# Kernel optimization log

Measured on AMD Instinct MI355X. Metric: run time of the kernel, lower is better.

## Reference

```python
import jax, jax.numpy as jnp
import numpy as np

N = 50000      # nodes
E = 800000     # edges (avg degree 16)
F_IN = 128
HID = 128
C = 40
EPS = 1e-5     # BatchNorm1d eps


def setup_inputs() -> dict:
    key = jax.random.key(0)
    ks = jax.random.split(key, 8)

    def glorot(k, shape):
        lim = np.sqrt(6.0 / (shape[0] + shape[1])).astype(np.float32)
        return jax.random.uniform(k, shape, jnp.float32, -lim, lim)

    inp = {
        "features": jax.random.normal(ks[0], (N, F_IN), jnp.float32),
        "edge_index": jax.random.randint(ks[1], (2, E), 0, N, jnp.int32),
        "W1": glorot(ks[2], (F_IN, HID)), "b1": jnp.zeros((HID,), jnp.float32),
        "gamma1": jnp.ones((HID,), jnp.float32), "beta1": jnp.zeros((HID,), jnp.float32),
        "W2": glorot(ks[3], (HID, HID)), "b2": jnp.zeros((HID,), jnp.float32),
        "gamma2": jnp.ones((HID,), jnp.float32), "beta2": jnp.zeros((HID,), jnp.float32),
        "W3": glorot(ks[4], (HID, C)), "b3": jnp.zeros((C,), jnp.float32),
    }
    return inp


def _gcn_norm(edge_index):
    # Add self-loops and compute symmetric normalization D^-1/2 (A+I) D^-1/2
    loops = jnp.arange(N, dtype=edge_index.dtype)
    src = jnp.concatenate([edge_index[0], loops])
    dst = jnp.concatenate([edge_index[1], loops])
    deg = jax.ops.segment_sum(jnp.ones((E + N,), jnp.float32), dst, num_segments=N)
    dinv = jax.lax.rsqrt(jnp.maximum(deg, 1.0))
    return src, dst, dinv[src] * dinv[dst]  # per-edge norm coefficient


def _gcn_conv(x, W, b, src, dst, norm):
    h = x @ W                                   # [N, out]
    msg = h[src] * norm[:, None]                # gather + scale, [E+N, out]
    return jax.ops.segment_sum(msg, dst, num_segments=N) + b


def _bn(x, gamma, beta):
    # training-mode BatchNorm1d over the node axis (biased variance)
    mu = jnp.mean(x, axis=0)
    var = jnp.mean(jnp.square(x - mu), axis=0)
    return (x - mu) * jax.lax.rsqrt(var + EPS) * gamma + beta


def reference(features, edge_index, W1, b1, gamma1, beta1, W2, b2, gamma2, beta2, W3, b3):
    src, dst, norm = _gcn_norm(edge_index)
    h = jax.nn.relu(_bn(_gcn_conv(features, W1, b1, src, dst, norm), gamma1, beta1))
    h = jax.nn.relu(_bn(_gcn_conv(h, W2, b2, src, dst, norm), gamma2, beta2))
    h = _gcn_conv(h, W3, b3, src, dst, norm)
    return jax.nn.log_softmax(h, axis=-1)
```

## Files before the change

kernel.cpp:

```cpp
#include <hip/hip_runtime.h>
#include <math.h>

#define FEAT 128
#define NCLS 40
#define BN_EPS 1e-5f
#define CAP 64

typedef unsigned short u16;
typedef unsigned int u32;
typedef __attribute__((ext_vector_type(8))) short bf16x8;
typedef __attribute__((ext_vector_type(4))) float f32x4;

__device__ inline u32 f2b2(float a, float b) {
    u32 ua = __float_as_uint(a), ub = __float_as_uint(b);
    ua = (ua + 0x7fffu + ((ua >> 16) & 1u)) >> 16;
    ub = (ub + 0x7fffu + ((ub >> 16) & 1u)) >> 16;
    return ua | (ub << 16);
}
__device__ inline u16 f2b1(float a) {
    u32 ua = __float_as_uint(a);
    return (u16)((ua + 0x7fffu + ((ua >> 16) & 1u)) >> 16);
}
__device__ inline float b2f(u16 u) { return __uint_as_float((u32)u << 16); }
__device__ inline float blo(u32 u) { return __uint_as_float(u << 16); }
__device__ inline float bhi(u32 u) { return __uint_as_float(u & 0xffff0000u); }

__device__ inline void b8acc(uint4 u, float w, float* a) {
    a[0] = fmaf(w, blo(u.x), a[0]); a[1] = fmaf(w, bhi(u.x), a[1]);
    a[2] = fmaf(w, blo(u.y), a[2]); a[3] = fmaf(w, bhi(u.y), a[3]);
    a[4] = fmaf(w, blo(u.z), a[4]); a[5] = fmaf(w, bhi(u.z), a[5]);
    a[6] = fmaf(w, blo(u.w), a[6]); a[7] = fmaf(w, bhi(u.w), a[7]);
}


__device__ inline void stage_wt(const float* __restrict__ W, u16* Wt) {
    const float4* W4 = (const float4*)W;
#pragma unroll
    for (int i = 0; i < 16; ++i) {
        int li = threadIdx.x + i * 256;
        int k = li >> 5;
        int n0 = (li & 31) * 4;
        int s = k >> 5, quad = (k >> 3) & 3, koff = k & 7;
        int nt = n0 >> 4, nl0 = n0 & 15;
        int base = ((s * 8 + nt) * 64 + quad * 16) * 8 + koff;
        float4 w = W4[li];
        Wt[base + (nl0 + 0) * 8] = f2b1(w.x);
        Wt[base + (nl0 + 1) * 8] = f2b1(w.y);
        Wt[base + (nl0 + 2) * 8] = f2b1(w.z);
        Wt[base + (nl0 + 3) * 8] = f2b1(w.w);
    }
}

__device__ inline void stage_wt40(const float* __restrict__ W, u16* Wt) {
    for (int e = threadIdx.x; e < 12 * 64 * 8; e += 256) {
        int j = e & 7;
        int lane = (e >> 3) & 63;
        int tile = e >> 9;
        int s = tile / 3, nt = tile % 3;
        int n = nt * 16 + (lane & 15);
        int k = s * 32 + (lane >> 4) * 8 + j;
        float v = (n < NCLS) ? W[k * NCLS + n] : 0.f;
        Wt[e] = f2b1(v);
    }
}

__global__ __launch_bounds__(256) void k_init(
    const float* __restrict__ W1, const float* __restrict__ W2,
    const float* __restrict__ W3, u16* __restrict__ Wg,
    uint4* __restrict__ zbase, int zcount, int zblocks,
    const int* __restrict__ edges, u16* __restrict__ ew, int twoE)
{
    int b = blockIdx.x;
    if (b == 0) stage_wt(W1, Wg);
    else if (b == 1) stage_wt(W2, Wg + 128 * 128);
    else if (b == 2) stage_wt40(W3, Wg + 2 * 128 * 128);
    else if (b < 3 + zblocks) {
        int idx = (b - 3) * 256 + threadIdx.x;
        if (idx < zcount) zbase[idx] = make_uint4(0, 0, 0, 0);
    } else {
        int idx = ((b - 3 - zblocks) * 256 + threadIdx.x) * 8;
        if (idx + 8 <= twoE) {
            int4 a = *(const int4*)(edges + idx);
            int4 c = *(const int4*)(edges + idx + 4);
            uint4 o;
            o.x = (u32)(a.x & 0xffff) | ((u32)a.y << 16);
            o.y = (u32)(a.z & 0xffff) | ((u32)a.w << 16);
            o.z = (u32)(c.x & 0xffff) | ((u32)c.y << 16);
            o.w = (u32)(c.z & 0xffff) | ((u32)c.w << 16);
            *(uint4*)(ew + idx) = o;
        } else {
            for (int e = idx; e < twoE; ++e) ew[e] = (u16)edges[e];
        }
    }
}

__device__ inline void mfma_core(const uint4* __restrict__ wt4, const bf16x8* bfrag,
                                 u16* __restrict__ Y, int node, int M, int nl, int quad) {
    int lane = quad * 16 + nl;
    f32x4 acc[8];
#pragma unroll
    for (int nt = 0; nt < 8; ++nt) acc[nt] = (f32x4){0.f, 0.f, 0.f, 0.f};
#pragma unroll
    for (int s = 0; s < 4; ++s) {
#pragma unroll
        for (int nt = 0; nt < 8; ++nt) {
            uint4 aw = wt4[(s * 8 + nt) * 64 + lane];
            bf16x8 af = *(bf16x8*)&aw;
            acc[nt] = __builtin_amdgcn_mfma_f32_16x16x32_bf16(af, bfrag[s], acc[nt], 0, 0, 0);
        }
    }
    if (node < M) {
#pragma unroll
        for (int nt = 0; nt < 8; ++nt) {
            uint2 o;
            o.x = f2b2(acc[nt][0], acc[nt][1]);
            o.y = f2b2(acc[nt][2], acc[nt][3]);
            *(uint2*)&Y[(size_t)node * 128 + nt * 16 + quad * 4] = o;
        }
    }
}


__global__ __launch_bounds__(256, 8) void k_l1_fill(
    const float* __restrict__ X, const u16* __restrict__ Wg, u16* __restrict__ Y, int M,
    const u16* __restrict__ srcw, const u16* __restrict__ dstw,
    int* __restrict__ cnt, u16* __restrict__ col, int E,
    int gemmBlocks, int nchunks)
{
    if ((int)blockIdx.x < gemmBlocks) {
        int wv = threadIdx.x >> 6;
        int lane = threadIdx.x & 63;
        int nl = lane & 15, quad = lane >> 4;
        int node = blockIdx.x * 64 + wv * 16 + nl;

        bf16x8 bfrag[4];
        if (node < M) {
            const float4* xr = (const float4*)(X + (size_t)node * 128);
#pragma unroll
            for (int s = 0; s < 4; ++s) {
                float4 xa = xr[s * 8 + quad * 2];
                float4 xb = xr[s * 8 + quad * 2 + 1];
                uint4 bu;
                bu.x = f2b2(xa.x, xa.y); bu.y = f2b2(xa.z, xa.w);
                bu.z = f2b2(xb.x, xb.y); bu.w = f2b2(xb.z, xb.w);
                bfrag[s] = *(bf16x8*)&bu;
            }
        } else {
            uint4 z = make_uint4(0, 0, 0, 0);
#pragma unroll
            for (int s = 0; s < 4; ++s) bfrag[s] = *(bf16x8*)&z;
        }
        mfma_core((const uint4*)Wg, bfrag, Y, node, M, nl, quad);
    } else {
        int fb = blockIdx.x - gemmBlocks;
        int part = fb & 7;
        int chunk = fb >> 3;
        int lo = (int)(((long long)M * part) >> 3);
        int hi = (int)(((long long)M * (part + 1)) >> 3);
        int per = ((E + nchunks - 1) / nchunks + 7) & ~7;
        int e0 = chunk * per;
        int e1 = e0 + per; if (e1 > E) e1 = E;

        for (int eb = e0 + (int)threadIdx.x * 8; eb < e1; eb += 2048) {
            if (eb + 8 <= e1) {
                uint4 du = *(const uint4*)(dstw + eb);
                uint4 su = *(const uint4*)(srcw + eb);
                int dd[8] = {(int)(du.x & 0xffffu), (int)(du.x >> 16),
                             (int)(du.y & 0xffffu), (int)(du.y >> 16),
                             (int)(du.z & 0xffffu), (int)(du.z >> 16),
                             (int)(du.w & 0xffffu), (int)(du.w >> 16)};
                u16 ss[8] = {(u16)(su.x & 0xffffu), (u16)(su.x >> 16),
                             (u16)(su.y & 0xffffu), (u16)(su.y >> 16),
                             (u16)(su.z & 0xffffu), (u16)(su.z >> 16),
                             (u16)(su.w & 0xffffu), (u16)(su.w >> 16)};
#pragma unroll
                for (int k = 0; k < 8; ++k) {
                    int d = dd[k];
                    if (d >= lo && d < hi) {
                        int c = atomicAdd(&cnt[d], 1);
                        if (c < CAP) col[(size_t)d * CAP + c] = ss[k];
                    }
                }
            } else {
                for (int e = eb; e < e1; ++e) {
                    int d = (int)dstw[e];
                    if (d >= lo && d < hi) {
                        int c = atomicAdd(&cnt[d], 1);
                        if (c < CAP) col[(size_t)d * CAP + c] = srcw[e];
                    }
                }
            }
        }
    }
}


__device__ inline void build_bfrag_bn(const u16* __restrict__ X, int node, int M,
                                      int quad, const float* scs, const float* shs,
                                      bf16x8* bfrag) {
    if (node < M) {
        const uint4* xr = (const uint4*)(X + (size_t)node * 128);
#pragma unroll
        for (int s = 0; s < 4; ++s) {
            int k0 = s * 32 + quad * 8;
            uint4 xu = xr[s * 4 + quad];
            float4 sc0 = *(const float4*)&scs[k0];
            float4 sc1 = *(const float4*)&scs[k0 + 4];
            float4 sh0 = *(const float4*)&shs[k0];
            float4 sh1 = *(const float4*)&shs[k0 + 4];
            float v0 = fmaxf(fmaf(blo(xu.x), sc0.x, sh0.x), 0.f);
            float v1 = fmaxf(fmaf(bhi(xu.x), sc0.y, sh0.y), 0.f);
            float v2 = fmaxf(fmaf(blo(xu.y), sc0.z, sh0.z), 0.f);
            float v3 = fmaxf(fmaf(bhi(xu.y), sc0.w, sh0.w), 0.f);
            float v4 = fmaxf(fmaf(blo(xu.z), sc1.x, sh1.x), 0.f);
            float v5 = fmaxf(fmaf(bhi(xu.z), sc1.y, sh1.y), 0.f);
            float v6 = fmaxf(fmaf(blo(xu.w), sc1.z, sh1.z), 0.f);
            float v7 = fmaxf(fmaf(bhi(xu.w), sc1.w, sh1.w), 0.f);
            uint4 bu;
            bu.x = f2b2(v0, v1); bu.y = f2b2(v2, v3);
            bu.z = f2b2(v4, v5); bu.w = f2b2(v6, v7);
            bfrag[s] = *(bf16x8*)&bu;
        }
    } else {
        uint4 z = make_uint4(0, 0, 0, 0);
#pragma unroll
        for (int s = 0; s < 4; ++s) bfrag[s] = *(bf16x8*)&z;
    }
}

__global__ __launch_bounds__(256, 2) void k_mfma_l2(
    const u16* __restrict__ X, const u16* __restrict__ Wg,
    const float* __restrict__ sums, const float* __restrict__ gamma,
    const float* __restrict__ beta, u16* __restrict__ Y, int M)
{
    __shared__ __align__(16) u16 Wt[128 * 128];
    __shared__ __align__(16) float scs[128], shs[128];

    if (threadIdx.x < 128) {
        int f = threadIdx.x;
        float inv_n = 1.f / (float)M;
        float mu = sums[f] * inv_n;
        float var = sums[128 + f] * inv_n - mu * mu;
        float rs = rsqrtf(var + BN_EPS);
        float sc = gamma[f] * rs;
        scs[f] = sc;
        shs[f] = beta[f] - mu * sc;
    }
    {
        uint4* d4 = (uint4*)Wt;
        const uint4* s4 = (const uint4*)Wg;
#pragma unroll
        for (int i = 0; i < 8; ++i) d4[threadIdx.x + i * 256] = s4[threadIdx.x + i * 256];
    }
    __syncthreads();

    int wv = threadIdx.x >> 6;
    int lane = threadIdx.x & 63;
    int nl = lane & 15, quad = lane >> 4;
    int nodeA = blockIdx.x * 128 + wv * 16 + nl;
    int nodeB = nodeA + 64;

    bf16x8 bfragA[4], bfragB[4];
    build_bfrag_bn(X, nodeA, M, quad, scs, shs, bfragA);
    build_bfrag_bn(X, nodeB, M, quad, scs, shs, bfragB);

    const uint4* wt4 = (const uint4*)Wt;
    f32x4 accA[8], accB[8];
#pragma unroll
    for (int nt = 0; nt < 8; ++nt) {
        accA[nt] = (f32x4){0.f, 0.f, 0.f, 0.f};
        accB[nt] = (f32x4){0.f, 0.f, 0.f, 0.f};
    }
#pragma unroll
    for (int s = 0; s < 4; ++s) {
#pragma unroll
        for (int nt = 0; nt < 8; ++nt) {
            uint4 aw = wt4[(s * 8 + nt) * 64 + lane];
            bf16x8 af = *(bf16x8*)&aw;
            accA[nt] = __builtin_amdgcn_mfma_f32_16x16x32_bf16(af, bfragA[s], accA[nt], 0, 0, 0);
            accB[nt] = __builtin_amdgcn_mfma_f32_16x16x32_bf16(af, bfragB[s], accB[nt], 0, 0, 0);
        }
    }
    if (nodeA < M) {
#pragma unroll
        for (int nt = 0; nt < 8; ++nt) {
            uint2 o;
            o.x = f2b2(accA[nt][0], accA[nt][1]);
            o.y = f2b2(accA[nt][2], accA[nt][3]);
            *(uint2*)&Y[(size_t)nodeA * 128 + nt * 16 + quad * 4] = o;
        }
    }
    if (nodeB < M) {
#pragma unroll
        for (int nt = 0; nt < 8; ++nt) {
            uint2 o;
            o.x = f2b2(accB[nt][0], accB[nt][1]);
            o.y = f2b2(accB[nt][2], accB[nt][3]);
            *(uint2*)&Y[(size_t)nodeB * 128 + nt * 16 + quad * 4] = o;
        }
    }
}


__global__ __launch_bounds__(256) void k_mfma_l3(
    const u16* __restrict__ X, const u16* __restrict__ Wg,
    const float* __restrict__ sums, const float* __restrict__ gamma,
    const float* __restrict__ beta, u16* __restrict__ Y, int M)
{
    __shared__ __align__(16) u16 Wt[12 * 64 * 8];
    __shared__ __align__(16) float scs[128], shs[128];

    if (threadIdx.x < 128) {
        int f = threadIdx.x;
        float inv_n = 1.f / (float)M;
        float mu = sums[f] * inv_n;
        float var = sums[128 + f] * inv_n - mu * mu;
        float rs = rsqrtf(var + BN_EPS);
        float sc = gamma[f] * rs;
        scs[f] = sc;
        shs[f] = beta[f] - mu * sc;
    }
    {
        uint4* d4 = (uint4*)Wt;
        const uint4* s4 = (const uint4*)Wg;
#pragma unroll
        for (int i = 0; i < 3; ++i) d4[threadIdx.x + i * 256] = s4[threadIdx.x + i * 256];
    }
    __syncthreads();

    int wv = threadIdx.x >> 6;
    int lane = threadIdx.x & 63;
    int nl = lane & 15, quad = lane >> 4;
    int node = blockIdx.x * 64 + wv * 16 + nl;

    bf16x8 bfrag[4];
    build_bfrag_bn(X, node, M, quad, scs, shs, bfrag);

    const uint4* wt4 = (const uint4*)Wt;
    f32x4 acc[3];
#pragma unroll
    for (int nt = 0; nt < 3; ++nt) acc[nt] = (f32x4){0.f, 0.f, 0.f, 0.f};
#pragma unroll
    for (int s = 0; s < 4; ++s) {
#pragma unroll
        for (int nt = 0; nt < 3; ++nt) {
            uint4 aw = wt4[(s * 3 + nt) * 64 + lane];
            bf16x8 af = *(bf16x8*)&aw;
            acc[nt] = __builtin_amdgcn_mfma_f32_16x16x32_bf16(af, bfrag[s], acc[nt], 0, 0, 0);
        }
    }
    if (node < M) {
#pragma unroll
        for (int nt = 0; nt < 3; ++nt) {
            int c0 = nt * 16 + quad * 4;
            if (c0 < NCLS) {
                uint2 o;
                o.x = f2b2(acc[nt][0], acc[nt][1]);
                o.y = f2b2(acc[nt][2], acc[nt][3]);
                *(uint2*)&Y[(size_t)node * NCLS + c0] = o;
            }
        }
    }
}


__global__ __launch_bounds__(256) void k_agg128_bn(
    const u16* __restrict__ t, const int* __restrict__ cnt,
    const u16* __restrict__ col, const float* __restrict__ bias,
    u16* __restrict__ out, float* __restrict__ sums, int n)
{
    int wid = threadIdx.x >> 4;
    int lane = threadIdx.x & 15;
    float4 bA = ((const float4*)bias)[lane * 2];
    float4 bB = ((const float4*)bias)[lane * 2 + 1];

    float bs[8], bq[8];
#pragma unroll
    for (int k = 0; k < 8; ++k) { bs[k] = 0.f; bq[k] = 0.f; }

    for (int i0 = blockIdx.x * 16; i0 < n; i0 += gridDim.x * 16) {
        int i = i0 + wid;
        if (i < n) {
            int c = cnt[i];
            int deg = c < CAP ? c : CAP;
            int beg = i * CAP, end = beg + deg;
            float di = rsqrtf((float)(c + 1));

            float a[8];
            {
                uint4 su = ((const uint4*)(t + (size_t)i * 128))[lane];
                a[0] = di * blo(su.x); a[1] = di * bhi(su.x);
                a[2] = di * blo(su.y); a[3] = di * bhi(su.y);
                a[4] = di * blo(su.z); a[5] = di * bhi(su.z);
                a[6] = di * blo(su.w); a[7] = di * bhi(su.w);
            }

            int j = beg;
            for (; j + 7 < end; j += 8) {
                int s[8]; int sc[8]; uint4 v[8];
#pragma unroll
                for (int k = 0; k < 8; ++k) s[k] = (int)col[j + k];
#pragma unroll
                for (int k = 0; k < 8; ++k) {
                    sc[k] = cnt[s[k]];
                    v[k] = ((const uint4*)(t + (size_t)s[k] * 128))[lane];
                }
#pragma unroll
                for (int k = 0; k < 8; ++k) b8acc(v[k], rsqrtf((float)(sc[k] + 1)), a);
            }
            for (; j < end; ++j) {
                int s0 = (int)col[j];
                float w0 = rsqrtf((float)(cnt[s0] + 1));
                uint4 v = ((const uint4*)(t + (size_t)s0 * 128))[lane];
                b8acc(v, w0, a);
            }

            float vv[8];
            vv[0] = fmaf(di, a[0], bA.x); vv[1] = fmaf(di, a[1], bA.y);
            vv[2] = fmaf(di, a[2], bA.z); vv[3] = fmaf(di, a[3], bA.w);
            vv[4] = fmaf(di, a[4], bB.x); vv[5] = fmaf(di, a[5], bB.y);
            vv[6] = fmaf(di, a[6], bB.z); vv[7] = fmaf(di, a[7], bB.w);
            uint4 o;
            o.x = f2b2(vv[0], vv[1]); o.y = f2b2(vv[2], vv[3]);
            o.z = f2b2(vv[4], vv[5]); o.w = f2b2(vv[6], vv[7]);
            ((uint4*)(out + (size_t)i * 128))[lane] = o;
#pragma unroll
            for (int k = 0; k < 8; ++k) {
                bs[k] += vv[k];
                bq[k] = fmaf(vv[k], vv[k], bq[k]);
            }
        }
    }

    __shared__ float red[16][128];
#pragma unroll
    for (int k = 0; k < 8; ++k) red[wid][lane * 8 + k] = bs[k];
    __syncthreads();
    if (threadIdx.x < 128) {
        float v = 0.f;
#pragma unroll
        for (int w = 0; w < 16; ++w) v += red[w][threadIdx.x];
        atomicAdd(&sums[threadIdx.x], v);
    }
    __syncthreads();
#pragma unroll
    for (int k = 0; k < 8; ++k) red[wid][lane * 8 + k] = bq[k];
    __syncthreads();
    if (threadIdx.x < 128) {
        float v = 0.f;
#pragma unroll
        for (int w = 0; w < 16; ++w) v += red[w][threadIdx.x];
        atomicAdd(&sums[128 + threadIdx.x], v);
    }
}


__global__ __launch_bounds__(256) void k_agg40(
    const u16* __restrict__ t, const int* __restrict__ cnt,
    const u16* __restrict__ col, const float* __restrict__ bias,
    float* __restrict__ out, int n)
{
    int i = blockIdx.x * 32 + (threadIdx.x >> 3);
    if (i >= n) return;
    int l = threadIdx.x & 7;
    bool act = l < 5;
    int c = cnt[i];
    int deg = c < CAP ? c : CAP;
    int beg = i * CAP, end = beg + deg;
    float di = rsqrtf((float)(c + 1));

    float a[8] = {0.f, 0.f, 0.f, 0.f, 0.f, 0.f, 0.f, 0.f};
    if (act) {
        uint4 su = ((const uint4*)(t + (size_t)i * NCLS))[l];
        a[0] = di * blo(su.x); a[1] = di * bhi(su.x);
        a[2] = di * blo(su.y); a[3] = di * bhi(su.y);
        a[4] = di * blo(su.z); a[5] = di * bhi(su.z);
        a[6] = di * blo(su.w); a[7] = di * bhi(su.w);
    }
    int j = beg;
    for (; j + 7 < end; j += 8) {
        int s[8]; int sc[8]; uint4 v[8];
#pragma unroll
        for (int k = 0; k < 8; ++k) s[k] = (int)col[j + k];
#pragma unroll
        for (int k = 0; k < 8; ++k) {
            sc[k] = cnt[s[k]];
            v[k] = act ? ((const uint4*)(t + (size_t)s[k] * NCLS))[l]
                       : make_uint4(0, 0, 0, 0);
        }
#pragma unroll
        for (int k = 0; k < 8; ++k) b8acc(v[k], rsqrtf((float)(sc[k] + 1)), a);
    }
    for (; j < end; ++j) {
        int s0 = (int)col[j];
        float w0 = rsqrtf((float)(cnt[s0] + 1));
        uint4 v = act ? ((const uint4*)(t + (size_t)s0 * NCLS))[l]
                      : make_uint4(0, 0, 0, 0);
        b8acc(v, w0, a);
    }

    float v[8];
    float m = -INFINITY;
    if (act) {
        float4 b0 = *(const float4*)(bias + l * 8);
        float4 b1 = *(const float4*)(bias + l * 8 + 4);
        v[0] = fmaf(di, a[0], b0.x); v[1] = fmaf(di, a[1], b0.y);
        v[2] = fmaf(di, a[2], b0.z); v[3] = fmaf(di, a[3], b0.w);
        v[4] = fmaf(di, a[4], b1.x); v[5] = fmaf(di, a[5], b1.y);
        v[6] = fmaf(di, a[6], b1.z); v[7] = fmaf(di, a[7], b1.w);
#pragma unroll
        for (int k = 0; k < 8; ++k) m = fmaxf(m, v[k]);
    }
#pragma unroll
    for (int d = 1; d < 8; d <<= 1) m = fmaxf(m, __shfl_xor(m, d, 8));
    float es = 0.f;
    if (act) {
#pragma unroll
        for (int k = 0; k < 8; ++k) es += expf(v[k] - m);
    }
#pragma unroll
    for (int d = 1; d < 8; d <<= 1) es += __shfl_xor(es, d, 8);
    float ls = logf(es);
    if (act) {
        float4 o0, o1;
        o0.x = v[0] - m - ls; o0.y = v[1] - m - ls;
        o0.z = v[2] - m - ls; o0.w = v[3] - m - ls;
        o1.x = v[4] - m - ls; o1.y = v[5] - m - ls;
        o1.z = v[6] - m - ls; o1.w = v[7] - m - ls;
        *(float4*)(out + (size_t)i * NCLS + l * 8) = o0;
        *(float4*)(out + (size_t)i * NCLS + l * 8 + 4) = o1;
    }
}


extern "C" void kernel_launch(void* const* d_in, const int* in_sizes, int n_in,
                              void* d_out, int out_size, void* d_ws, size_t ws_size,
                              hipStream_t stream) {
    const float* features = (const float*)d_in[0];
    const int* edge_index = (const int*)d_in[1];
    const float* W1 = (const float*)d_in[2];
    const float* b1 = (const float*)d_in[3];
    const float* gamma1 = (const float*)d_in[4];
    const float* beta1 = (const float*)d_in[5];
    const float* W2 = (const float*)d_in[6];
    const float* b2 = (const float*)d_in[7];
    const float* gamma2 = (const float*)d_in[8];
    const float* beta2 = (const float*)d_in[9];
    const float* W3 = (const float*)d_in[10];
    const float* b3 = (const float*)d_in[11];
    float* out = (float*)d_out;

    int n = in_sizes[0] / FEAT;
    int E = in_sizes[1] / 2;

    char* p = (char*)d_ws;
    auto alloc = [&](size_t bytes) -> void* {
        void* r = (void*)p;
        p += (bytes + 255) & ~(size_t)255;
        return r;
    };
    int* cnt     = (int*)alloc((size_t)n * 4);
    float* sums  = (float*)alloc(512 * 4);
    size_t zspan = (size_t)((char*)(sums + 512) - (char*)cnt);
    u16* colb    = (u16*)alloc((size_t)n * CAP * 2);
    u16* hb      = (u16*)alloc((size_t)n * 128 * 2);
    u16* ab      = (u16*)alloc((size_t)n * 128 * 2);
    u16* wgb     = (u16*)alloc((size_t)(2 * 128 * 128 + 12 * 64 * 8) * 2);
    u16* ew      = (u16*)alloc((size_t)2 * E * 2);

    float* sums1 = sums;
    float* sums2 = sums + 256;
    u16* Wg1 = wgb;
    u16* Wg2 = wgb + 128 * 128;
    u16* Wg3 = wgb + 2 * 128 * 128;
    u16* srcw = ew;
    u16* dstw = ew + E;

    int gb64 = (n + 63) / 64;
    int gb128 = (n + 127) / 128;
    int gb16 = (n + 15) / 16;
    int gb32 = (n + 31) / 32;
    int aggGrid = gb16 < 1024 ? gb16 : 1024;

    int zcount = (int)(zspan / 16);
    int zblocks = (zcount + 255) / 256;
    int twoE = 2 * E;
    int cblocks = (twoE / 8 + 255) / 256;
    k_init<<<3 + zblocks + cblocks, 256, 0, stream>>>(W1, W2, W3, wgb,
                                                      (uint4*)cnt, zcount, zblocks,
                                                      edge_index, ew, twoE);

    int nchunks = 160;
    k_l1_fill<<<gb64 + nchunks * 8, 256, 0, stream>>>(features, Wg1, hb, n,
                                                      srcw, dstw, cnt, colb, E,
                                                      gb64, nchunks);

    k_agg128_bn<<<aggGrid, 256, 0, stream>>>(hb, cnt, colb, b1, ab, sums1, n);

    k_mfma_l2<<<gb128, 256, 0, stream>>>(ab, Wg2, sums1, gamma1, beta1, hb, n);
    k_agg128_bn<<<aggGrid, 256, 0, stream>>>(hb, cnt, colb, b2, ab, sums2, n);

    k_mfma_l3<<<gb64, 256, 0, stream>>>(ab, Wg3, sums2, gamma2, beta2, hb, n);
    k_agg40<<<gb32, 256, 0, stream>>>(hb, cnt, colb, b3, out, n);
}
```

Measured before the change: 298.6 us.

## Partition aggregation into XCD-local node ranges and batch neighbor-index loads

Both aggregation kernels now map each block to one of eight contiguous node partitions, selected by blockIdx mod 8. The apparent aim is that blocks on the same XCD work on nearby nodes, improving L2 locality for cnt and column reads. The gather loop loads 16 neighbor indices per iteration as two vector loads and unrolls 16 row gathers to raise memory-level parallelism. The tail is handled with masked 8-wide vector loads, which needs 64 bytes of padding on the column buffer. k_agg40 becomes a persistent grid-stride kernel with 512 blocks, and launch bounds now request 4 blocks per CU, which risks register pressure from the 16-deep unroll.

```diff
diff --git a/kernel.cpp b/kernel.cpp
--- a/kernel.cpp
+++ b/kernel.cpp
@@ -364,7 +364,7 @@
 }
 
 
-__global__ __launch_bounds__(256) void k_agg128_bn(
+__global__ __launch_bounds__(256, 4) void k_agg128_bn(
     const u16* __restrict__ t, const int* __restrict__ cnt,
     const u16* __restrict__ col, const float* __restrict__ bias,
     u16* __restrict__ out, float* __restrict__ sums, int n)
@@ -378,9 +378,15 @@
 #pragma unroll
     for (int k = 0; k < 8; ++k) { bs[k] = 0.f; bq[k] = 0.f; }
 
-    for (int i0 = blockIdx.x * 16; i0 < n; i0 += gridDim.x * 16) {
+    int part = blockIdx.x & 7;
+    int bslot = blockIdx.x >> 3;
+    int nb = gridDim.x >> 3;
+    int plo = (int)(((long long)n * part) >> 3);
+    int phi = (int)(((long long)n * (part + 1)) >> 3);
+
+    for (int i0 = plo + bslot * 16; i0 < phi; i0 += nb * 16) {
         int i = i0 + wid;
-        if (i < n) {
+        if (i < phi) {
             int c = cnt[i];
             int deg = c < CAP ? c : CAP;
             int beg = i * CAP, end = beg + deg;
@@ -396,23 +402,45 @@
             }
 
             int j = beg;
-            for (; j + 7 < end; j += 8) {
-                int s[8]; int sc[8]; uint4 v[8];
-#pragma unroll
-                for (int k = 0; k < 8; ++k) s[k] = (int)col[j + k];
-#pragma unroll
-                for (int k = 0; k < 8; ++k) {
+            for (; j + 15 < end; j += 16) {
+                uint4 c0 = *(const uint4*)(col + j);
+                uint4 c1 = *(const uint4*)(col + j + 8);
+                int s[16] = {
+                    (int)(c0.x & 0xffffu), (int)(c0.x >> 16),
+                    (int)(c0.y & 0xffffu), (int)(c0.y >> 16),
+                    (int)(c0.z & 0xffffu), (int)(c0.z >> 16),
+                    (int)(c0.w & 0xffffu), (int)(c0.w >> 16),
+                    (int)(c1.x & 0xffffu), (int)(c1.x >> 16),
+                    (int)(c1.y & 0xffffu), (int)(c1.y >> 16),
+                    (int)(c1.z & 0xffffu), (int)(c1.z >> 16),
+                    (int)(c1.w & 0xffffu), (int)(c1.w >> 16)};
+                int sc[16]; uint4 v[16];
+#pragma unroll
+                for (int k = 0; k < 16; ++k) {
                     sc[k] = cnt[s[k]];
                     v[k] = ((const uint4*)(t + (size_t)s[k] * 128))[lane];
                 }
 #pragma unroll
-                for (int k = 0; k < 8; ++k) b8acc(v[k], rsqrtf((float)(sc[k] + 1)), a);
-            }
-            for (; j < end; ++j) {
-                int s0 = (int)col[j];
-                float w0 = rsqrtf((float)(cnt[s0] + 1));
-                uint4 v = ((const uint4*)(t + (size_t)s0 * 128))[lane];
-                b8acc(v, w0, a);
+                for (int k = 0; k < 16; ++k) b8acc(v[k], rsqrtf((float)(sc[k] + 1)), a);
+            }
+            for (; j < end; j += 8) {
+                uint4 c0 = *(const uint4*)(col + j);
+                int sr[8] = {
+                    (int)(c0.x & 0xffffu), (int)(c0.x >> 16),
+                    (int)(c0.y & 0xffffu), (int)(c0.y >> 16),
+                    (int)(c0.z & 0xffffu), (int)(c0.z >> 16),
+                    (int)(c0.w & 0xffffu), (int)(c0.w >> 16)};
+                float w[8]; uint4 v[8];
+#pragma unroll
+                for (int k = 0; k < 8; ++k) {
+                    bool valid = (j + k) < end;
+                    int s = valid ? sr[k] : 0;
+                    int sck = cnt[s];
+                    v[k] = ((const uint4*)(t + (size_t)s * 128))[lane];
+                    w[k] = valid ? rsqrtf((float)(sck + 1)) : 0.f;
+                }
+#pragma unroll
+                for (int k = 0; k < 8; ++k) b8acc(v[k], w[k], a);
             }
 
             float vv[8];
@@ -455,80 +483,110 @@
 }
 
 
-__global__ __launch_bounds__(256) void k_agg40(
+__global__ __launch_bounds__(256, 4) void k_agg40(
     const u16* __restrict__ t, const int* __restrict__ cnt,
     const u16* __restrict__ col, const float* __restrict__ bias,
     float* __restrict__ out, int n)
 {
-    int i = blockIdx.x * 32 + (threadIdx.x >> 3);
-    if (i >= n) return;
+    int wid = threadIdx.x >> 3;
     int l = threadIdx.x & 7;
     bool act = l < 5;
-    int c = cnt[i];
-    int deg = c < CAP ? c : CAP;
-    int beg = i * CAP, end = beg + deg;
-    float di = rsqrtf((float)(c + 1));
-
-    float a[8] = {0.f, 0.f, 0.f, 0.f, 0.f, 0.f, 0.f, 0.f};
-    if (act) {
-        uint4 su = ((const uint4*)(t + (size_t)i * NCLS))[l];
-        a[0] = di * blo(su.x); a[1] = di * bhi(su.x);
-        a[2] = di * blo(su.y); a[3] = di * bhi(su.y);
-        a[4] = di * blo(su.z); a[5] = di * bhi(su.z);
-        a[6] = di * blo(su.w); a[7] = di * bhi(su.w);
-    }
-    int j = beg;
-    for (; j + 7 < end; j += 8) {
-        int s[8]; int sc[8]; uint4 v[8];
-#pragma unroll
-        for (int k = 0; k < 8; ++k) s[k] = (int)col[j + k];
-#pragma unroll
-        for (int k = 0; k < 8; ++k) {
-            sc[k] = cnt[s[k]];
-            v[k] = act ? ((const uint4*)(t + (size_t)s[k] * NCLS))[l]
-                       : make_uint4(0, 0, 0, 0);
-        }
-#pragma unroll
-        for (int k = 0; k < 8; ++k) b8acc(v[k], rsqrtf((float)(sc[k] + 1)), a);
-    }
-    for (; j < end; ++j) {
-        int s0 = (int)col[j];
-        float w0 = rsqrtf((float)(cnt[s0] + 1));
-        uint4 v = act ? ((const uint4*)(t + (size_t)s0 * NCLS))[l]
-                      : make_uint4(0, 0, 0, 0);
-        b8acc(v, w0, a);
-    }
-
-    float v[8];
-    float m = -INFINITY;
-    if (act) {
-        float4 b0 = *(const float4*)(bias + l * 8);
-        float4 b1 = *(const float4*)(bias + l * 8 + 4);
-        v[0] = fmaf(di, a[0], b0.x); v[1] = fmaf(di, a[1], b0.y);
-        v[2] = fmaf(di, a[2], b0.z); v[3] = fmaf(di, a[3], b0.w);
-        v[4] = fmaf(di, a[4], b1.x); v[5] = fmaf(di, a[5], b1.y);
-        v[6] = fmaf(di, a[6], b1.z); v[7] = fmaf(di, a[7], b1.w);
-#pragma unroll
-        for (int k = 0; k < 8; ++k) m = fmaxf(m, v[k]);
-    }
-#pragma unroll
-    for (int d = 1; d < 8; d <<= 1) m = fmaxf(m, __shfl_xor(m, d, 8));
-    float es = 0.f;
-    if (act) {
-#pragma unroll
-        for (int k = 0; k < 8; ++k) es += expf(v[k] - m);
-    }
-#pragma unroll
-    for (int d = 1; d < 8; d <<= 1) es += __shfl_xor(es, d, 8);
-    float ls = logf(es);
-    if (act) {
-        float4 o0, o1;
-        o0.x = v[0] - m - ls; o0.y = v[1] - m - ls;
-        o0.z = v[2] - m - ls; o0.w = v[3] - m - ls;
-        o1.x = v[4] - m - ls; o1.y = v[5] - m - ls;
-        o1.z = v[6] - m - ls; o1.w = v[7] - m - ls;
-        *(float4*)(out + (size_t)i * NCLS + l * 8) = o0;
-        *(float4*)(out + (size_t)i * NCLS + l * 8 + 4) = o1;
+
+    int part = blockIdx.x & 7;
+    int bslot = blockIdx.x >> 3;
+    int nb = gridDim.x >> 3;
+    int plo = (int)(((long long)n * part) >> 3);
+    int phi = (int)(((long long)n * (part + 1)) >> 3);
+
+    for (int i0 = plo + bslot * 32; i0 < phi; i0 += nb * 32) {
+        int i = i0 + wid;
+        if (i >= phi) continue;
+        int c = cnt[i];
+        int deg = c < CAP ? c : CAP;
+        int beg = i * CAP, end = beg + deg;
+        float di = rsqrtf((float)(c + 1));
+
+        float a[8] = {0.f, 0.f, 0.f, 0.f, 0.f, 0.f, 0.f, 0.f};
+        if (act) {
+            uint4 su = ((const uint4*)(t + (size_t)i * NCLS))[l];
+            a[0] = di * blo(su.x); a[1] = di * bhi(su.x);
+            a[2] = di * blo(su.y); a[3] = di * bhi(su.y);
+            a[4] = di * blo(su.z); a[5] = di * bhi(su.z);
+            a[6] = di * blo(su.w); a[7] = di * bhi(su.w);
+        }
+        int j = beg;
+        for (; j + 15 < end; j += 16) {
+            uint4 c0 = *(const uint4*)(col + j);
+            uint4 c1 = *(const uint4*)(col + j + 8);
+            int s[16] = {
+                (int)(c0.x & 0xffffu), (int)(c0.x >> 16),
+                (int)(c0.y & 0xffffu), (int)(c0.y >> 16),
+                (int)(c0.z & 0xffffu), (int)(c0.z >> 16),
+                (int)(c0.w & 0xffffu), (int)(c0.w >> 16),
+                (int)(c1.x & 0xffffu), (int)(c1.x >> 16),
+                (int)(c1.y & 0xffffu), (int)(c1.y >> 16),
+                (int)(c1.z & 0xffffu), (int)(c1.z >> 16),
+                (int)(c1.w & 0xffffu), (int)(c1.w >> 16)};
+            int sc[16]; uint4 v[16];
+#pragma unroll
+            for (int k = 0; k < 16; ++k) {
+                sc[k] = cnt[s[k]];
+                v[k] = act ? ((const uint4*)(t + (size_t)s[k] * NCLS))[l]
+                           : make_uint4(0, 0, 0, 0);
+            }
+#pragma unroll
+            for (int k = 0; k < 16; ++k) b8acc(v[k], rsqrtf((float)(sc[k] + 1)), a);
+        }
+        for (; j < end; j += 8) {
+            uint4 c0 = *(const uint4*)(col + j);
+            int sr[8] = {
+                (int)(c0.x & 0xffffu), (int)(c0.x >> 16),
+                (int)(c0.y & 0xffffu), (int)(c0.y >> 16),
+                (int)(c0.z & 0xffffu), (int)(c0.z >> 16),
+                (int)(c0.w & 0xffffu), (int)(c0.w >> 16)};
+#pragma unroll
+            for (int k = 0; k < 8; ++k) {
+                bool valid = (j + k) < end;
+                int s = valid ? sr[k] : 0;
+                int sck = cnt[s];
+                uint4 v = act ? ((const uint4*)(t + (size_t)s * NCLS))[l]
+                              : make_uint4(0, 0, 0, 0);
+                float w = valid ? rsqrtf((float)(sck + 1)) : 0.f;
+                b8acc(v, w, a);
+            }
+        }
+
+        float v[8];
+        float m = -INFINITY;
+        if (act) {
+            float4 b0 = *(const float4*)(bias + l * 8);
+            float4 b1 = *(const float4*)(bias + l * 8 + 4);
+            v[0] = fmaf(di, a[0], b0.x); v[1] = fmaf(di, a[1], b0.y);
+            v[2] = fmaf(di, a[2], b0.z); v[3] = fmaf(di, a[3], b0.w);
+            v[4] = fmaf(di, a[4], b1.x); v[5] = fmaf(di, a[5], b1.y);
+            v[6] = fmaf(di, a[6], b1.z); v[7] = fmaf(di, a[7], b1.w);
+#pragma unroll
+            for (int k = 0; k < 8; ++k) m = fmaxf(m, v[k]);
+        }
+#pragma unroll
+        for (int d = 1; d < 8; d <<= 1) m = fmaxf(m, __shfl_xor(m, d, 8));
+        float es = 0.f;
+        if (act) {
+#pragma unroll
+            for (int k = 0; k < 8; ++k) es += expf(v[k] - m);
+        }
+#pragma unroll
+        for (int d = 1; d < 8; d <<= 1) es += __shfl_xor(es, d, 8);
+        float ls = logf(es);
+        if (act) {
+            float4 o0, o1;
+            o0.x = v[0] - m - ls; o0.y = v[1] - m - ls;
+            o0.z = v[2] - m - ls; o0.w = v[3] - m - ls;
+            o1.x = v[4] - m - ls; o1.y = v[5] - m - ls;
+            o1.z = v[6] - m - ls; o1.w = v[7] - m - ls;
+            *(float4*)(out + (size_t)i * NCLS + l * 8) = o0;
+            *(float4*)(out + (size_t)i * NCLS + l * 8 + 4) = o1;
+        }
     }
 }
 
@@ -562,7 +620,7 @@
     int* cnt     = (int*)alloc((size_t)n * 4);
     float* sums  = (float*)alloc(512 * 4);
     size_t zspan = (size_t)((char*)(sums + 512) - (char*)cnt);
-    u16* colb    = (u16*)alloc((size_t)n * CAP * 2);
+    u16* colb    = (u16*)alloc((size_t)n * CAP * 2 + 64);
     u16* hb      = (u16*)alloc((size_t)n * 128 * 2);
     u16* ab      = (u16*)alloc((size_t)n * 128 * 2);
     u16* wgb     = (u16*)alloc((size_t)(2 * 128 * 128 + 12 * 64 * 8) * 2);
@@ -579,8 +637,9 @@
     int gb64 = (n + 63) / 64;
     int gb128 = (n + 127) / 128;
     int gb16 = (n + 15) / 16;
-    int gb32 = (n + 31) / 32;
-    int aggGrid = gb16 < 1024 ? gb16 : 1024;
+    int aggGrid = 1024;
+    if (gb16 * 2 < aggGrid) aggGrid = ((gb16 + 7) / 8) * 8;
+    int agg40Grid = 512;
 
     int zcount = (int)(zspan / 16);
     int zblocks = (zcount + 255) / 256;
@@ -601,5 +660,5 @@
     k_agg128_bn<<<aggGrid, 256, 0, stream>>>(hb, cnt, colb, b2, ab, sums2, n);
 
     k_mfma_l3<<<gb64, 256, 0, stream>>>(ab, Wg3, sums2, gamma2, beta2, hb, n);
-    k_agg40<<<gb32, 256, 0, stream>>>(hb, cnt, colb, b3, out, n);
-}
+    k_agg40<<<agg40Grid, 256, 0, stream>>>(hb, cnt, colb, b3, out, n);
+}
```

After: 342.7 us. 14.8% more time.
